# Performance work log

Measured on AMD Instinct MI355X. Metric: run time of the kernel, lower is better.

The kernel has to match this reference:

```python
import jax, jax.numpy as jnp
import numpy as np

B, T, E, C = 64, 512, 768, 20


def setup_inputs() -> dict:
    key = jax.random.key(0)
    ks = jax.random.split(key, 8)
    hidden = jax.random.normal(ks[0], (B, T, E), jnp.float32)
    attention_mask = jnp.ones((B, T), jnp.int32)
    labels = jax.random.randint(ks[1], (B, T), 0, C)
    fc_w = jax.random.normal(ks[2], (C, E), jnp.float32) * 0.02
    fc_b = jnp.zeros((C,), jnp.float32)
    # torchcrf initializes transitions ~ Uniform(-0.1, 0.1)
    start_transitions = jax.random.uniform(ks[3], (C,), jnp.float32, -0.1, 0.1)
    end_transitions = jax.random.uniform(ks[4], (C,), jnp.float32, -0.1, 0.1)
    transitions = jax.random.uniform(ks[5], (C, C), jnp.float32, -0.1, 0.1)
    return {"hidden": hidden, "attention_mask": attention_mask, "labels": labels,
            "fc_w": fc_w, "fc_b": fc_b, "start_transitions": start_transitions,
            "end_transitions": end_transitions, "transitions": transitions}


def _crf_log_likelihood(emissions, tags, mask, start_t, end_t, trans):
    # emissions [B,T,C], tags [B,T] int, mask [B,T]
    Bn = emissions.shape[0]
    emT = jnp.swapaxes(emissions, 0, 1)            # [T,B,C]
    tagsT = jnp.swapaxes(tags, 0, 1)               # [T,B]
    maskT = jnp.swapaxes(mask, 0, 1).astype(emissions.dtype)  # [T,B]
    barange = jnp.arange(Bn)
    # --- numerator: score of the gold path ---
    score = start_t[tagsT[0]] + emT[0, barange, tagsT[0]]
    def num_step(s, x):
        em_t, tag_t, tag_p, m_t = x
        s = s + (trans[tag_p, tag_t] + em_t[barange, tag_t]) * m_t
        return s, None
    score, _ = jax.lax.scan(num_step, score, (emT[1:], tagsT[1:], tagsT[:-1], maskT[1:]))
    seq_ends = jnp.sum(mask, axis=1).astype(jnp.int32) - 1
    last_tags = tags[barange, seq_ends]
    score = score + end_t[last_tags]
    # --- denominator: forward algorithm (logsumexp recurrence) ---
    alpha = start_t[None, :] + emT[0]              # [B,C]
    def den_step(a, x):
        em_t, m_t = x
        nxt = jax.nn.logsumexp(a[:, :, None] + trans[None, :, :] + em_t[:, None, :], axis=1)
        a = jnp.where(m_t[:, None] > 0, nxt, a)
        return a, None
    alpha, _ = jax.lax.scan(den_step, alpha, (emT[1:], maskT[1:]))
    norm = jax.nn.logsumexp(alpha + end_t[None, :], axis=1)
    return score - norm


def _viterbi_decode(emissions, mask, start_t, end_t, trans):
    emT = jnp.swapaxes(emissions, 0, 1)            # [T,B,C]
    maskT = jnp.swapaxes(mask, 0, 1)               # [T,B]
    alpha = start_t[None, :] + emT[0]              # [B,C]
    def step(a, x):
        em_t, m_t = x
        sc = a[:, :, None] + trans[None, :, :]     # [B, prev C, cur C]
        best = jnp.max(sc, axis=1) + em_t
        idx = jnp.argmax(sc, axis=1)               # [B,C] best prev tag
        a2 = jnp.where(m_t[:, None] > 0, best, a)
        return a2, idx
    alpha, hist = jax.lax.scan(step, alpha, (emT[1:], maskT[1:]))  # hist [T-1,B,C]
    last = jnp.argmax(alpha + end_t[None, :], axis=1)  # [B]
    def back(tag, idx_t):
        prev = jnp.take_along_axis(idx_t, tag[:, None], axis=1)[:, 0]
        return prev, prev
    _, prevs = jax.lax.scan(back, last, hist, reverse=True)  # [T-1,B]
    path = jnp.concatenate([jnp.swapaxes(prevs, 0, 1), last[:, None]], axis=1)  # [B,T]
    return path


def reference(hidden, attention_mask, labels, fc_w, fc_b, start_transitions, end_transitions, transitions):
    # linear head on BERT hidden states -> per-token emissions
    emissions = jnp.einsum('bte,ce->btc', hidden, fc_w) + fc_b
    llh = _crf_log_likelihood(emissions, labels, attention_mask,
                              start_transitions, end_transitions, transitions)
    loss = -jnp.mean(llh)  # crf(..., reduction='mean') negated
    path = _viterbi_decode(emissions, attention_mask, start_transitions,
                           end_transitions, transitions) + 1  # res_paths = x + 1
    return (loss, path)
```

## Files before the change

### kernel.cpp

```cpp
#include <hip/hip_runtime.h>
#include <hip/hip_bf16.h>

#define BB 64
#define TT 512
#define EE 768
#define CC 20
#define MID 256

typedef __attribute__((ext_vector_type(8))) short bf16x8;
typedef __attribute__((ext_vector_type(4))) float f32x4;

__device__ __forceinline__ float rlane(float x, int l) {
  return __int_as_float(__builtin_amdgcn_readlane(__float_as_int(x), l));
}
__device__ __forceinline__ short f2bf(float x) {
  union { __hip_bfloat16 h; short s; } u;
  u.h = __float2bfloat16(x);
  return u.s;
}
__device__ __forceinline__ bf16x8 pack8(float4 a, float4 b) {
  bf16x8 r;
  r[0] = f2bf(a.x); r[1] = f2bf(a.y); r[2] = f2bf(a.z); r[3] = f2bf(a.w);
  r[4] = f2bf(b.x); r[5] = f2bf(b.y); r[6] = f2bf(b.z); r[7] = f2bf(b.w);
  return r;
}

__global__ __launch_bounds__(256) void packw_kernel(const float* __restrict__ fc_w,
                                                    short* __restrict__ wfrag) {
  int t = blockIdx.x * 256 + threadIdx.x;
  int lane = t & 63;
  int kc = (t >> 6) % 24;
  int tile = t / (24 * 64);
  int n = tile * 16 + (lane & 15);
  if (n >= CC) n = CC - 1;
  int k0 = kc * 32 + (lane >> 4) * 8;
  const float* src = fc_w + (size_t)n * EE + k0;
  float4 x = *(const float4*)src;
  float4 y = *(const float4*)(src + 4);
  ((bf16x8*)wfrag)[t] = pack8(x, y);
}

__global__ __launch_bounds__(256) void emissions_kernel(
    const float* __restrict__ hidden, const short* __restrict__ wfrag,
    const float* __restrict__ fc_b, float* __restrict__ em) {
  __shared__ short wsh[2 * 24 * 64 * 8];
  {
    const int4* src = (const int4*)wfrag;
    int4* dst = (int4*)wsh;
    for (int i = threadIdx.x; i < 3072; i += 256) dst[i] = src[i];
  }
  __syncthreads();
  const int wave = threadIdx.x >> 6;
  const int lane = threadIdx.x & 63;
  const int token0 = blockIdx.x * 64 + wave * 16;
  const int m = lane & 15, q = lane >> 4;
  const float* hrow = hidden + (size_t)(token0 + m) * EE + q * 8;
  const bf16x8* wp = (const bf16x8*)wsh;
  f32x4 acc0 = {0.f, 0.f, 0.f, 0.f}, acc1 = {0.f, 0.f, 0.f, 0.f};
#pragma unroll 4
  for (int kb = 0; kb < 24; ++kb) {
    float4 a0 = *(const float4*)(hrow + kb * 32);
    float4 a1 = *(const float4*)(hrow + kb * 32 + 4);
    bf16x8 Ab = pack8(a0, a1);
    bf16x8 w0 = wp[kb * 64 + lane];
    bf16x8 w1 = wp[(24 + kb) * 64 + lane];
    acc0 = __builtin_amdgcn_mfma_f32_16x16x32_bf16(Ab, w0, acc0, 0, 0, 0);
    acc1 = __builtin_amdgcn_mfma_f32_16x16x32_bf16(Ab, w1, acc1, 0, 0, 0);
  }
  const int col = lane & 15;
  const float b0v = fc_b[col];
  const bool has1 = (16 + col < CC);
  const float b1v = has1 ? fc_b[16 + col] : 0.f;
#pragma unroll
  for (int r = 0; r < 4; ++r) {
    int tok = token0 + q * 4 + r;
    em[(size_t)tok * CC + col] = acc0[r] + b0v;
    if (has1) em[(size_t)tok * CC + 16 + col] = acc1[r] + b1v;
  }
}

#define VDECL(Q) float v##Q = rlane(a, Q) + tv[Q]; int j##Q = Q;
#define MRG(A_, B_) { bool k_ = (v##A_ >= v##B_); v##A_ = k_ ? v##A_ : v##B_; j##A_ = k_ ? j##A_ : j##B_; }
__device__ __forceinline__ void vstep(float a, const float (&tv)[CC], float& vm, int& jm) {
  VDECL(0) VDECL(1) VDECL(2) VDECL(3) VDECL(4) VDECL(5) VDECL(6) VDECL(7)
  VDECL(8) VDECL(9) VDECL(10) VDECL(11) VDECL(12) VDECL(13) VDECL(14)
  VDECL(15) VDECL(16) VDECL(17) VDECL(18) VDECL(19)
  MRG(0, 10) MRG(1, 11) MRG(2, 12) MRG(3, 13) MRG(4, 14)
  MRG(5, 15) MRG(6, 16) MRG(7, 17) MRG(8, 18) MRG(9, 19)
  MRG(0, 5) MRG(1, 6) MRG(2, 7) MRG(3, 8) MRG(4, 9)
  MRG(0, 1) MRG(2, 3)
  MRG(0, 2) MRG(0, 4)
  vm = v0; jm = j0;
}
#define XDECL(Q) float x##Q = rlane(x, Q); int y##Q = Q;
#define MRX(A_, B_) { bool k_ = (x##A_ >= x##B_); x##A_ = k_ ? x##A_ : x##B_; y##A_ = k_ ? y##A_ : y##B_; }
__device__ __forceinline__ int lane_argmax(float x) {
  XDECL(0) XDECL(1) XDECL(2) XDECL(3) XDECL(4) XDECL(5) XDECL(6) XDECL(7)
  XDECL(8) XDECL(9) XDECL(10) XDECL(11) XDECL(12) XDECL(13) XDECL(14)
  XDECL(15) XDECL(16) XDECL(17) XDECL(18) XDECL(19)
  MRX(0, 10) MRX(1, 11) MRX(2, 12) MRX(3, 13) MRX(4, 14)
  MRX(5, 15) MRX(6, 16) MRX(7, 17) MRX(8, 18) MRX(9, 19)
  MRX(0, 5) MRX(1, 6) MRX(2, 7) MRX(3, 8) MRX(4, 9)
  MRX(0, 1) MRX(2, 3)
  MRX(0, 2) MRX(0, 4)
  return y0;
}

__device__ __forceinline__ float fdot(float Es, const float (&ET)[CC]) {
  float s0 = rlane(Es, 0) * ET[0];
  float s1 = rlane(Es, 1) * ET[1];
  float s2 = rlane(Es, 2) * ET[2];
  float s3 = rlane(Es, 3) * ET[3];
  s0 = fmaf(rlane(Es, 4), ET[4], s0);
  s1 = fmaf(rlane(Es, 5), ET[5], s1);
  s2 = fmaf(rlane(Es, 6), ET[6], s2);
  s3 = fmaf(rlane(Es, 7), ET[7], s3);
  s0 = fmaf(rlane(Es, 8), ET[8], s0);
  s1 = fmaf(rlane(Es, 9), ET[9], s1);
  s2 = fmaf(rlane(Es, 10), ET[10], s2);
  s3 = fmaf(rlane(Es, 11), ET[11], s3);
  s0 = fmaf(rlane(Es, 12), ET[12], s0);
  s1 = fmaf(rlane(Es, 13), ET[13], s1);
  s2 = fmaf(rlane(Es, 14), ET[14], s2);
  s3 = fmaf(rlane(Es, 15), ET[15], s3);
  s0 = fmaf(rlane(Es, 16), ET[16], s0);
  s1 = fmaf(rlane(Es, 17), ET[17], s1);
  s2 = fmaf(rlane(Es, 18), ET[18], s2);
  s3 = fmaf(rlane(Es, 19), ET[19], s3);
  return (s0 + s1) + (s2 + s3);
}

__global__ __launch_bounds__(64) void crf_half_kernel(
    const float* __restrict__ em, const int* __restrict__ mask,
    const float* __restrict__ st, const float* __restrict__ en,
    const float* __restrict__ tr,
    float* __restrict__ amw, float* __restrict__ bmw,
    float* __restrict__ avw, float* __restrict__ bvw,
    unsigned char* __restrict__ bpws, unsigned char* __restrict__ fpws) {
  __shared__ float emsh[(MID + 1) * CC];
  __shared__ int msh[TT];
  const int tid = threadIdx.x;
  const int quad = blockIdx.x >> 6;
  const int b = blockIdx.x & (BB - 1);
  const int back = quad & 1;
  const int cc = tid < CC ? tid : CC - 1;
  const float K = 1.44269504088896340736f;

  {
    const float* base = em + (size_t)b * TT * CC + (back ? MID * CC : 0);
    int nf4 = back ? (MID * CC / 4) : ((MID + 1) * CC / 4);
    const float4* src = (const float4*)base;
    float4* dst = (float4*)emsh;
    for (int i = tid; i < nf4; i += 64) dst[i] = src[i];
    for (int i = tid; i < TT; i += 64) msh[i] = mask[b * TT + i];
  }
  __syncthreads();

  if (quad == 0) {
    float ET[CC];
#pragma unroll
    for (int q = 0; q < CC; ++q) ET[q] = __builtin_amdgcn_exp2f(tr[q * CC + cc] * K);
    float r = st[cc] + emsh[cc];
    float base0 = rlane(r, 0);
    float Es = __builtin_amdgcn_exp2f((r - base0) * K);
    float off = base0 * K;
    int ie = 0;
    float emc = emsh[CC + cc];
    int mcur = msh[1];
    float eec = __builtin_amdgcn_exp2f(emc * K);
    for (int t = 1; t <= MID; ++t) {
      int tn = (t < MID) ? t + 1 : t;
      float emn = emsh[tn * CC + cc];
      int mn = msh[tn];
      float s = fdot(Es, ET) * eec;
      Es = mcur ? s : Es;
      if ((t & 7) == 0) {
        float p = rlane(Es, 0);
        int e = ((__float_as_int(p) >> 23) & 255) - 127;
        Es *= __int_as_float((127 - e) << 23);
        ie += e;
      }
      eec = __builtin_amdgcn_exp2f(emn * K);
      mcur = mn;
    }
    if (tid < CC) amw[b * CC + tid] = off + (float)ie + __builtin_amdgcn_logf(Es);
  } else if (quad == 1) {
    float ETr[CC];
#pragma unroll
    for (int q = 0; q < CC; ++q) ETr[q] = __builtin_amdgcn_exp2f(tr[cc * CC + q] * K);
    const float ENc = __builtin_amdgcn_exp2f(en[cc] * K);
    float Bs = ENc;
    int ie = 0;
    float em1 = emsh[(TT - 1 - MID) * CC + cc];
    int m1 = msh[TT - 1];
    float ee1 = __builtin_amdgcn_exp2f(em1 * K);
    for (int t = TT - 2; t >= MID; --t) {
      float emn = emsh[(t - MID) * CC + cc];
      int mn = msh[t];
      float G = Bs * ee1;
      float s = fdot(G, ETr);
      Bs = m1 ? s : ENc;
      ie = m1 ? ie : 0;
      if ((t & 7) == 0) {
        float p = rlane(Bs, 0);
        int e = ((__float_as_int(p) >> 23) & 255) - 127;
        Bs *= __int_as_float((127 - e) << 23);
        ie += e;
      }
      ee1 = __builtin_amdgcn_exp2f(emn * K);
      m1 = mn;
    }
    if (tid < CC) bmw[b * CC + tid] = (float)ie + __builtin_amdgcn_logf(Bs);
  } else if (quad == 2) {
    float tv[CC];
#pragma unroll
    for (int q = 0; q < CC; ++q) tv[q] = tr[q * CC + cc];
    float a = st[cc] + emsh[cc];
    float emc = emsh[CC + cc];
    int mcur = msh[1];
    unsigned char* bp = bpws + (size_t)b * MID * CC;
    for (int t = 1; t <= MID; ++t) {
      int tn = (t < MID) ? t + 1 : t;
      float emn = emsh[tn * CC + cc];
      int mn = msh[tn];
      float vm;
      int jm;
      vstep(a, tv, vm, jm);
      if (tid < CC) bp[(t - 1) * CC + tid] = (unsigned char)jm;
      float au = vm + emc;
      a = mcur ? au : a;
      emc = emn;
      mcur = mn;
    }
    if (tid < CC) avw[b * CC + tid] = a;
  } else {
    float tv[CC];
#pragma unroll
    for (int q = 0; q < CC; ++q) tv[q] = tr[cc * CC + q];
    const float ENv = en[cc];
    float Vb = ENv;
    float em1 = emsh[(TT - 1 - MID) * CC + cc];
    int m1 = msh[TT - 1];
    unsigned char* fp = fpws + (size_t)b * MID * CC;
    for (int t = TT - 2; t >= MID; --t) {
      float emn = emsh[(t - MID) * CC + cc];
      int mn = msh[t];
      float a = Vb + em1;
      float vm;
      int jm;
      vstep(a, tv, vm, jm);
      if (tid < CC) fp[(t - MID) * CC + tid] = (unsigned char)jm;
      Vb = m1 ? vm : ENv;
      em1 = emn;
      m1 = mn;
    }
    if (tid < CC) bvw[b * CC + tid] = Vb;
  }
}

__global__ __launch_bounds__(64) void finish_kernel(
    const float* __restrict__ em, const int* __restrict__ mask,
    const int* __restrict__ labels, const float* __restrict__ st,
    const float* __restrict__ en, const float* __restrict__ tr,
    const float* __restrict__ amw, const float* __restrict__ bmw,
    const float* __restrict__ avw, const float* __restrict__ bvw,
    const unsigned char* __restrict__ bpws, const unsigned char* __restrict__ fpws,
    float* __restrict__ llh, float* __restrict__ out) {
  __shared__ unsigned char hl[2 * MID * CC];
  const int b = blockIdx.x;
  const int tid = threadIdx.x;
  const int cc = tid < CC ? tid : CC - 1;
  const float LN2 = 0.69314718055994530942f;
  {
    const int4* bsrc = (const int4*)(bpws + (size_t)b * MID * CC);
    const int4* fsrc = (const int4*)(fpws + (size_t)b * MID * CC);
    int4* dst = (int4*)hl;
    for (int i = tid; i < 320; i += 64) {
      dst[i] = bsrc[i];
      dst[320 + i] = fsrc[i];
    }
  }
  __syncthreads();

  int cstar = lane_argmax(avw[b * CC + cc] + bvw[b * CC + cc]);
  float* ob = out + 1 + (size_t)b * TT;
  if (tid == 0) ob[MID] = (float)(cstar + 1);
  {
    int tag = cstar;
    int s = MID - 1;
    while (s >= 7) {
      int g0 = hl[(s - 0) * CC + cc];
      int g1 = hl[(s - 1) * CC + cc];
      int g2 = hl[(s - 2) * CC + cc];
      int g3 = hl[(s - 3) * CC + cc];
      int g4 = hl[(s - 4) * CC + cc];
      int g5 = hl[(s - 5) * CC + cc];
      int g6 = hl[(s - 6) * CC + cc];
      int g7 = hl[(s - 7) * CC + cc];
      tag = __builtin_amdgcn_readlane(g0, tag); float f0 = (float)(tag + 1);
      tag = __builtin_amdgcn_readlane(g1, tag); float f1 = (float)(tag + 1);
      tag = __builtin_amdgcn_readlane(g2, tag); float f2 = (float)(tag + 1);
      tag = __builtin_amdgcn_readlane(g3, tag); float f3 = (float)(tag + 1);
      tag = __builtin_amdgcn_readlane(g4, tag); float f4 = (float)(tag + 1);
      tag = __builtin_amdgcn_readlane(g5, tag); float f5 = (float)(tag + 1);
      tag = __builtin_amdgcn_readlane(g6, tag); float f6 = (float)(tag + 1);
      tag = __builtin_amdgcn_readlane(g7, tag); float f7 = (float)(tag + 1);
      if (tid == 0) {
        ob[s - 0] = f0; ob[s - 1] = f1; ob[s - 2] = f2; ob[s - 3] = f3;
        ob[s - 4] = f4; ob[s - 5] = f5; ob[s - 6] = f6; ob[s - 7] = f7;
      }
      s -= 8;
    }
  }
  {
    int tag = cstar;
    int u = 0;
    while (u + 7 <= MID - 2) {
      int g0 = hl[MID * CC + (u + 0) * CC + cc];
      int g1 = hl[MID * CC + (u + 1) * CC + cc];
      int g2 = hl[MID * CC + (u + 2) * CC + cc];
      int g3 = hl[MID * CC + (u + 3) * CC + cc];
      int g4 = hl[MID * CC + (u + 4) * CC + cc];
      int g5 = hl[MID * CC + (u + 5) * CC + cc];
      int g6 = hl[MID * CC + (u + 6) * CC + cc];
      int g7 = hl[MID * CC + (u + 7) * CC + cc];
      tag = __builtin_amdgcn_readlane(g0, tag); float f0 = (float)(tag + 1);
      tag = __builtin_amdgcn_readlane(g1, tag); float f1 = (float)(tag + 1);
      tag = __builtin_amdgcn_readlane(g2, tag); float f2 = (float)(tag + 1);
      tag = __builtin_amdgcn_readlane(g3, tag); float f3 = (float)(tag + 1);
      tag = __builtin_amdgcn_readlane(g4, tag); float f4 = (float)(tag + 1);
      tag = __builtin_amdgcn_readlane(g5, tag); float f5 = (float)(tag + 1);
      tag = __builtin_amdgcn_readlane(g6, tag); float f6 = (float)(tag + 1);
      tag = __builtin_amdgcn_readlane(g7, tag); float f7 = (float)(tag + 1);
      if (tid == 0) {
        ob[MID + 1 + u + 0] = f0; ob[MID + 1 + u + 1] = f1;
        ob[MID + 1 + u + 2] = f2; ob[MID + 1 + u + 3] = f3;
        ob[MID + 1 + u + 4] = f4; ob[MID + 1 + u + 5] = f5;
        ob[MID + 1 + u + 6] = f6; ob[MID + 1 + u + 7] = f7;
      }
      u += 8;
    }
    while (u <= MID - 2) {
      int g = hl[MID * CC + u * CC + cc];
      tag = __builtin_amdgcn_readlane(g, tag);
      if (tid == 0) ob[MID + 1 + u] = (float)(tag + 1);
      ++u;
    }
  }

  float zn = amw[b * CC + cc] + bmw[b * CC + cc];
  float M = zn;
#pragma unroll
  for (int o = 32; o >= 1; o >>= 1) M = fmaxf(M, __shfl_xor(M, o));
  float sE = (tid < CC) ? __builtin_amdgcn_exp2f(zn - M) : 0.f;
#pragma unroll
  for (int o = 32; o >= 1; o >>= 1) sE += __shfl_xor(sE, o);
  float norm = LN2 * (M + __builtin_amdgcn_logf(sE));

  const int* lab = labels + b * TT;
  const float* emg = em + (size_t)b * TT * CC;
  float sc = 0.f;
  int msum = 0;
  for (int k = tid; k < TT; k += 64) {
    int mk = mask[b * TT + k];
    msum += mk;
    if (k >= 1) {
      int tg = lab[k], tp = lab[k - 1];
      sc += (tr[tp * CC + tg] + emg[k * CC + tg]) * (float)mk;
    }
  }
#pragma unroll
  for (int o = 32; o >= 1; o >>= 1) {
    sc += __shfl_xor(sc, o);
    msum += __shfl_xor(msum, o);
  }
  int seq_end = msum - 1;
  int t0 = lab[0], tl = lab[seq_end];
  float score = sc + st[t0] + emg[t0] + en[tl];
  if (tid == 0) llh[b] = score - norm;
}

__global__ __launch_bounds__(64) void loss_kernel(const float* __restrict__ llh,
                                                  float* __restrict__ out) {
  float v = llh[threadIdx.x];
#pragma unroll
  for (int o = 32; o >= 1; o >>= 1) v += __shfl_xor(v, o);
  if (threadIdx.x == 0) out[0] = -(v * (1.0f / 64.0f));
}

extern "C" void kernel_launch(void* const* d_in, const int* in_sizes, int n_in,
                              void* d_out, int out_size, void* d_ws, size_t ws_size,
                              hipStream_t stream) {
  const float* hidden = (const float*)d_in[0];
  const int* amask = (const int*)d_in[1];
  const int* labels = (const int*)d_in[2];
  const float* fc_w = (const float*)d_in[3];
  const float* fc_b = (const float*)d_in[4];
  const float* st = (const float*)d_in[5];
  const float* en = (const float*)d_in[6];
  const float* tr = (const float*)d_in[7];

  float* emws = (float*)d_ws;
  float* llh = emws + (size_t)BB * TT * CC;
  short* wfrag = (short*)(llh + 64);
  float* amw = (float*)(wfrag + 24576);
  float* bmw = amw + BB * CC;
  float* avw = bmw + BB * CC;
  float* bvw = avw + BB * CC;
  unsigned char* bpws = (unsigned char*)(bvw + BB * CC);
  unsigned char* fpws = bpws + (size_t)BB * MID * CC;
  float* out = (float*)d_out;

  packw_kernel<<<(2 * 24 * 64) / 256, 256, 0, stream>>>(fc_w, wfrag);
  emissions_kernel<<<(BB * TT) / 64, 256, 0, stream>>>(hidden, wfrag, fc_b, emws);
  crf_half_kernel<<<4 * BB, 64, 0, stream>>>(emws, amask, st, en, tr,
                                             amw, bmw, avw, bvw, bpws, fpws);
  finish_kernel<<<BB, 64, 0, stream>>>(emws, amask, labels, st, en, tr,
                                       amw, bmw, avw, bvw, bpws, fpws, llh, out);
  loss_kernel<<<1, 64, 0, stream>>>(llh, out);
}
```

Before: 261.0 us.

## Block CRF recurrences by 8 steps with prefetch and packed backpointer layout

The forward and backward CRF and Viterbi recurrences now process 8 timesteps per block. Emission exponentials and masks for the next block are prefetched into registers, and renormalization runs once per block instead of being checked every step. Viterbi backpointers are packed eight per 64-bit word in a new [block][tag][8] layout, so each lane does one wide store and the backtrace reads one int2 per 8 steps instead of 8 byte loads. The emissions kernel drops its LDS staging of weights and reads the packed fragments straight from global memory. Costs are higher register pressure, a layout that the backtrace indexing must match exactly, and possibly worse weight-fetch locality.

```diff
diff --git a/kernel.cpp b/kernel.cpp
--- a/kernel.cpp
+++ b/kernel.cpp
@@ -43,19 +43,12 @@
 __global__ __launch_bounds__(256) void emissions_kernel(
     const float* __restrict__ hidden, const short* __restrict__ wfrag,
     const float* __restrict__ fc_b, float* __restrict__ em) {
-  __shared__ short wsh[2 * 24 * 64 * 8];
-  {
-    const int4* src = (const int4*)wfrag;
-    int4* dst = (int4*)wsh;
-    for (int i = threadIdx.x; i < 3072; i += 256) dst[i] = src[i];
-  }
-  __syncthreads();
   const int wave = threadIdx.x >> 6;
   const int lane = threadIdx.x & 63;
   const int token0 = blockIdx.x * 64 + wave * 16;
   const int m = lane & 15, q = lane >> 4;
   const float* hrow = hidden + (size_t)(token0 + m) * EE + q * 8;
-  const bf16x8* wp = (const bf16x8*)wsh;
+  const bf16x8* wp = (const bf16x8*)wfrag;
   f32x4 acc0 = {0.f, 0.f, 0.f, 0.f}, acc1 = {0.f, 0.f, 0.f, 0.f};
 #pragma unroll 4
   for (int kb = 0; kb < 24; ++kb) {
@@ -130,6 +123,14 @@
   return (s0 + s1) + (s2 + s3);
 }
 
+#define RENORM(Xs, iev)                                        \
+  {                                                            \
+    float p_ = rlane(Xs, 0);                                   \
+    int e_ = ((__float_as_int(p_) >> 23) & 255) - 127;         \
+    Xs *= __int_as_float((127 - e_) << 23);                    \
+    iev += e_;                                                 \
+  }
+
 __global__ __launch_bounds__(64) void crf_half_kernel(
     const float* __restrict__ em, const int* __restrict__ mask,
     const float* __restrict__ st, const float* __restrict__ en,
@@ -137,7 +138,7 @@
     float* __restrict__ amw, float* __restrict__ bmw,
     float* __restrict__ avw, float* __restrict__ bvw,
     unsigned char* __restrict__ bpws, unsigned char* __restrict__ fpws) {
-  __shared__ float emsh[(MID + 1) * CC];
+  __shared__ __align__(16) float emsh[(MID + 1) * CC];
   __shared__ int msh[TT];
   const int tid = threadIdx.x;
   const int quad = blockIdx.x >> 6;
@@ -148,11 +149,15 @@
 
   {
     const float* base = em + (size_t)b * TT * CC + (back ? MID * CC : 0);
-    int nf4 = back ? (MID * CC / 4) : ((MID + 1) * CC / 4);
     const float4* src = (const float4*)base;
     float4* dst = (float4*)emsh;
-    for (int i = tid; i < nf4; i += 64) dst[i] = src[i];
-    for (int i = tid; i < TT; i += 64) msh[i] = mask[b * TT + i];
+#pragma unroll
+    for (int k = 0; k < 21; ++k) {
+      int i = tid + k * 64;
+      if (i < 1285) dst[i] = src[i];
+    }
+#pragma unroll
+    for (int k = 0; k < 8; ++k) msh[tid + k * 64] = mask[b * TT + tid + k * 64];
   }
   __syncthreads();
 
@@ -165,23 +170,28 @@
     float Es = __builtin_amdgcn_exp2f((r - base0) * K);
     float off = base0 * K;
     int ie = 0;
-    float emc = emsh[CC + cc];
-    int mcur = msh[1];
-    float eec = __builtin_amdgcn_exp2f(emc * K);
-    for (int t = 1; t <= MID; ++t) {
-      int tn = (t < MID) ? t + 1 : t;
-      float emn = emsh[tn * CC + cc];
-      int mn = msh[tn];
-      float s = fdot(Es, ET) * eec;
-      Es = mcur ? s : Es;
-      if ((t & 7) == 0) {
-        float p = rlane(Es, 0);
-        int e = ((__float_as_int(p) >> 23) & 255) - 127;
-        Es *= __int_as_float((127 - e) << 23);
-        ie += e;
-      }
-      eec = __builtin_amdgcn_exp2f(emn * K);
-      mcur = mn;
+    float eev[8]; int mv[8];
+#pragma unroll
+    for (int i = 0; i < 8; ++i) {
+      eev[i] = __builtin_amdgcn_exp2f(emsh[(1 + i) * CC + cc] * K);
+      mv[i] = msh[1 + i];
+    }
+    for (int j = 0; j < 32; ++j) {
+      const int tb = (j < 31) ? 8 * j + 9 : 1;
+      float emn[8]; int mn[8];
+#pragma unroll
+      for (int i = 0; i < 8; ++i) { emn[i] = emsh[(tb + i) * CC + cc]; mn[i] = msh[tb + i]; }
+#pragma unroll
+      for (int i = 0; i < 8; ++i) {
+        float s = fdot(Es, ET) * eev[i];
+        Es = mv[i] ? s : Es;
+      }
+      RENORM(Es, ie)
+#pragma unroll
+      for (int i = 0; i < 8; ++i) {
+        eev[i] = __builtin_amdgcn_exp2f(emn[i] * K);
+        mv[i] = mn[i];
+      }
     }
     if (tid < CC) amw[b * CC + tid] = off + (float)ie + __builtin_amdgcn_logf(Es);
   } else if (quad == 1) {
@@ -191,24 +201,47 @@
     const float ENc = __builtin_amdgcn_exp2f(en[cc] * K);
     float Bs = ENc;
     int ie = 0;
-    float em1 = emsh[(TT - 1 - MID) * CC + cc];
+    float ee1 = __builtin_amdgcn_exp2f(emsh[255 * CC + cc] * K);
     int m1 = msh[TT - 1];
-    float ee1 = __builtin_amdgcn_exp2f(em1 * K);
-    for (int t = TT - 2; t >= MID; --t) {
-      float emn = emsh[(t - MID) * CC + cc];
+#pragma unroll
+    for (int k = 0; k < 7; ++k) {
+      const int t = 510 - k;
+      float emn = emsh[(t - 256) * CC + cc];
       int mn = msh[t];
       float G = Bs * ee1;
       float s = fdot(G, ETr);
       Bs = m1 ? s : ENc;
       ie = m1 ? ie : 0;
-      if ((t & 7) == 0) {
-        float p = rlane(Bs, 0);
-        int e = ((__float_as_int(p) >> 23) & 255) - 127;
-        Bs *= __int_as_float((127 - e) << 23);
-        ie += e;
-      }
       ee1 = __builtin_amdgcn_exp2f(emn * K);
       m1 = mn;
+    }
+    RENORM(Bs, ie)
+    float eev[8]; int mv[8];
+#pragma unroll
+    for (int i = 0; i < 8; ++i) {
+      eev[i] = __builtin_amdgcn_exp2f(emsh[(247 - i) * CC + cc] * K);
+      mv[i] = msh[503 - i];
+    }
+    for (int j = 0; j < 31; ++j) {
+      const int rb = (j < 30) ? (239 - 8 * j) : 247;
+      float emn[8]; int mn[8];
+#pragma unroll
+      for (int i = 0; i < 8; ++i) { emn[i] = emsh[(rb - i) * CC + cc]; mn[i] = msh[rb + 256 - i]; }
+#pragma unroll
+      for (int i = 0; i < 8; ++i) {
+        float G = Bs * ee1;
+        float s = fdot(G, ETr);
+        Bs = m1 ? s : ENc;
+        ie = m1 ? ie : 0;
+        ee1 = eev[i];
+        m1 = mv[i];
+      }
+      RENORM(Bs, ie)
+#pragma unroll
+      for (int i = 0; i < 8; ++i) {
+        eev[i] = __builtin_amdgcn_exp2f(emn[i] * K);
+        mv[i] = mn[i];
+      }
     }
     if (tid < CC) bmw[b * CC + tid] = (float)ie + __builtin_amdgcn_logf(Bs);
   } else if (quad == 2) {
@@ -216,21 +249,30 @@
 #pragma unroll
     for (int q = 0; q < CC; ++q) tv[q] = tr[q * CC + cc];
     float a = st[cc] + emsh[cc];
-    float emc = emsh[CC + cc];
-    int mcur = msh[1];
     unsigned char* bp = bpws + (size_t)b * MID * CC;
-    for (int t = 1; t <= MID; ++t) {
-      int tn = (t < MID) ? t + 1 : t;
-      float emn = emsh[tn * CC + cc];
-      int mn = msh[tn];
-      float vm;
-      int jm;
-      vstep(a, tv, vm, jm);
-      if (tid < CC) bp[(t - 1) * CC + tid] = (unsigned char)jm;
-      float au = vm + emc;
-      a = mcur ? au : a;
-      emc = emn;
-      mcur = mn;
+    float emv[8]; int mv[8];
+#pragma unroll
+    for (int i = 0; i < 8; ++i) { emv[i] = emsh[(1 + i) * CC + cc]; mv[i] = msh[1 + i]; }
+    for (int j = 0; j < 32; ++j) {
+      const int tb = (j < 31) ? 8 * j + 9 : 1;
+      float emn[8]; int mn[8];
+#pragma unroll
+      for (int i = 0; i < 8; ++i) { emn[i] = emsh[(tb + i) * CC + cc]; mn[i] = msh[tb + i]; }
+      unsigned lo = 0, hi = 0;
+#pragma unroll
+      for (int i = 0; i < 8; ++i) {
+        float vm; int jm;
+        vstep(a, tv, vm, jm);
+        if (i < 4) lo |= (unsigned)jm << (8 * i); else hi |= (unsigned)jm << (8 * (i - 4));
+        float au = vm + emv[i];
+        a = mv[i] ? au : a;
+      }
+      if (tid < CC) {
+        int2 w; w.x = (int)lo; w.y = (int)hi;
+        *(int2*)(bp + j * 160 + tid * 8) = w;
+      }
+#pragma unroll
+      for (int i = 0; i < 8; ++i) { emv[i] = emn[i]; mv[i] = mn[i]; }
     }
     if (tid < CC) avw[b * CC + tid] = a;
   } else {
@@ -239,20 +281,56 @@
     for (int q = 0; q < CC; ++q) tv[q] = tr[cc * CC + q];
     const float ENv = en[cc];
     float Vb = ENv;
-    float em1 = emsh[(TT - 1 - MID) * CC + cc];
+    float em1 = emsh[255 * CC + cc];
     int m1 = msh[TT - 1];
     unsigned char* fp = fpws + (size_t)b * MID * CC;
-    for (int t = TT - 2; t >= MID; --t) {
-      float emn = emsh[(t - MID) * CC + cc];
-      int mn = msh[t];
-      float a = Vb + em1;
-      float vm;
-      int jm;
-      vstep(a, tv, vm, jm);
-      if (tid < CC) fp[(t - MID) * CC + tid] = (unsigned char)jm;
-      Vb = m1 ? vm : ENv;
-      em1 = emn;
-      m1 = mn;
+    {
+      unsigned lo = 0, hi = 0;
+#pragma unroll
+      for (int k = 0; k < 7; ++k) {
+        const int t = 510 - k;
+        float emn = emsh[(t - 256) * CC + cc];
+        int mn = msh[t];
+        float av = Vb + em1;
+        float vm; int jm;
+        vstep(av, tv, vm, jm);
+        const int ib = 6 - k;
+        if (ib < 4) lo |= (unsigned)jm << (8 * ib); else hi |= (unsigned)jm << (8 * (ib - 4));
+        Vb = m1 ? vm : ENv;
+        em1 = emn;
+        m1 = mn;
+      }
+      if (tid < CC) {
+        int2 w; w.x = (int)lo; w.y = (int)hi;
+        *(int2*)(fp + 31 * 160 + tid * 8) = w;
+      }
+    }
+    float emv[8]; int mv[8];
+#pragma unroll
+    for (int i = 0; i < 8; ++i) { emv[i] = emsh[(247 - i) * CC + cc]; mv[i] = msh[503 - i]; }
+    for (int j = 0; j < 31; ++j) {
+      const int rb = (j < 30) ? (239 - 8 * j) : 247;
+      float emn[8]; int mn[8];
+#pragma unroll
+      for (int i = 0; i < 8; ++i) { emn[i] = emsh[(rb - i) * CC + cc]; mn[i] = msh[rb + 256 - i]; }
+      unsigned lo = 0, hi = 0;
+#pragma unroll
+      for (int i = 0; i < 8; ++i) {
+        float av = Vb + em1;
+        float vm; int jm;
+        vstep(av, tv, vm, jm);
+        const int ib = 7 - i;
+        if (ib < 4) lo |= (unsigned)jm << (8 * ib); else hi |= (unsigned)jm << (8 * (ib - 4));
+        Vb = m1 ? vm : ENv;
+        em1 = emv[i];
+        m1 = mv[i];
+      }
+      if (tid < CC) {
+        int2 w; w.x = (int)lo; w.y = (int)hi;
+        *(int2*)(fp + (30 - j) * 160 + tid * 8) = w;
+      }
+#pragma unroll
+      for (int i = 0; i < 8; ++i) { emv[i] = emn[i]; mv[i] = mn[i]; }
     }
     if (tid < CC) bvw[b * CC + tid] = Vb;
   }
@@ -266,7 +344,7 @@
     const float* __restrict__ avw, const float* __restrict__ bvw,
     const unsigned char* __restrict__ bpws, const unsigned char* __restrict__ fpws,
     float* __restrict__ llh, float* __restrict__ out) {
-  __shared__ unsigned char hl[2 * MID * CC];
+  __shared__ __align__(16) unsigned char hl[2 * MID * CC];
   const int b = blockIdx.x;
   const int tid = threadIdx.x;
   const int cc = tid < CC ? tid : CC - 1;
@@ -275,7 +353,9 @@
     const int4* bsrc = (const int4*)(bpws + (size_t)b * MID * CC);
     const int4* fsrc = (const int4*)(fpws + (size_t)b * MID * CC);
     int4* dst = (int4*)hl;
-    for (int i = tid; i < 320; i += 64) {
+#pragma unroll
+    for (int k = 0; k < 5; ++k) {
+      int i = tid + k * 64;
       dst[i] = bsrc[i];
       dst[320 + i] = fsrc[i];
     }
@@ -289,14 +369,10 @@
     int tag = cstar;
     int s = MID - 1;
     while (s >= 7) {
-      int g0 = hl[(s - 0) * CC + cc];
-      int g1 = hl[(s - 1) * CC + cc];
-      int g2 = hl[(s - 2) * CC + cc];
-      int g3 = hl[(s - 3) * CC + cc];
-      int g4 = hl[(s - 4) * CC + cc];
-      int g5 = hl[(s - 5) * CC + cc];
-      int g6 = hl[(s - 6) * CC + cc];
-      int g7 = hl[(s - 7) * CC + cc];
+      const unsigned char* hb = hl + (s >> 3) * 160 + cc * 8;
+      int2 w = *(const int2*)hb;
+      int g0 = (w.y >> 24) & 255, g1 = (w.y >> 16) & 255, g2 = (w.y >> 8) & 255, g3 = w.y & 255;
+      int g4 = (w.x >> 24) & 255, g5 = (w.x >> 16) & 255, g6 = (w.x >> 8) & 255, g7 = w.x & 255;
       tag = __builtin_amdgcn_readlane(g0, tag); float f0 = (float)(tag + 1);
       tag = __builtin_amdgcn_readlane(g1, tag); float f1 = (float)(tag + 1);
       tag = __builtin_amdgcn_readlane(g2, tag); float f2 = (float)(tag + 1);
@@ -316,14 +392,10 @@
     int tag = cstar;
     int u = 0;
     while (u + 7 <= MID - 2) {
-      int g0 = hl[MID * CC + (u + 0) * CC + cc];
-      int g1 = hl[MID * CC + (u + 1) * CC + cc];
-      int g2 = hl[MID * CC + (u + 2) * CC + cc];
-      int g3 = hl[MID * CC + (u + 3) * CC + cc];
-      int g4 = hl[MID * CC + (u + 4) * CC + cc];
-      int g5 = hl[MID * CC + (u + 5) * CC + cc];
-      int g6 = hl[MID * CC + (u + 6) * CC + cc];
-      int g7 = hl[MID * CC + (u + 7) * CC + cc];
+      const unsigned char* hb = hl + MID * CC + (u >> 3) * 160 + cc * 8;
+      int2 w = *(const int2*)hb;
+      int g0 = w.x & 255, g1 = (w.x >> 8) & 255, g2 = (w.x >> 16) & 255, g3 = (w.x >> 24) & 255;
+      int g4 = w.y & 255, g5 = (w.y >> 8) & 255, g6 = (w.y >> 16) & 255, g7 = (w.y >> 24) & 255;
       tag = __builtin_amdgcn_readlane(g0, tag); float f0 = (float)(tag + 1);
       tag = __builtin_amdgcn_readlane(g1, tag); float f1 = (float)(tag + 1);
       tag = __builtin_amdgcn_readlane(g2, tag); float f2 = (float)(tag + 1);
@@ -341,7 +413,7 @@
       u += 8;
     }
     while (u <= MID - 2) {
-      int g = hl[MID * CC + u * CC + cc];
+      int g = hl[MID * CC + (u >> 3) * 160 + cc * 8 + (u & 7)];
       tag = __builtin_amdgcn_readlane(g, tag);
       if (tid == 0) ob[MID + 1 + u] = (float)(tag + 1);
       ++u;
```

Measured after the change: 290.5 us. +11.3%, slower.
